# Performance work log

Measured on AMD Instinct MI355X. Metric: run time of the kernel, lower is better.

The kernel has to match this reference:

```python
import jax, jax.numpy as jnp
import numpy as np
from jax import lax

N_GRAPHS = 256
N_NODES = 128      # nodes per graph (fixed-size batching)
N_TPLT = 16
N_TPLT_NODES = 10
N_FEAT = 128
AVG_DEG = 8
EPS = 0.1          # entropic regularization for the GW solver
OUTER_ITERS = 5    # outer mirror-descent (entropic GW) iterations
SINKHORN_ITERS = 20


def setup_inputs() -> dict:
    key = jax.random.key(0)
    k1, k2, k3, k4, k5 = jax.random.split(key, 5)
    x = jax.random.normal(k1, (N_GRAPHS * N_NODES, N_FEAT), jnp.float32)
    # per-graph random edges with global node ids (PyG convention)
    n_e = N_NODES * AVG_DEG
    src = jax.random.randint(k2, (N_GRAPHS, n_e), 0, N_NODES)
    dst = jax.random.randint(k3, (N_GRAPHS, n_e), 0, N_NODES)
    off = (jnp.arange(N_GRAPHS) * N_NODES)[:, None]
    edge_index = jnp.stack([(src + off).reshape(-1), (dst + off).reshape(-1)]).astype(jnp.int32)
    batch = jnp.repeat(jnp.arange(N_GRAPHS, dtype=jnp.int32), N_NODES)
    # template parameters (symmetric uniform adjacencies, normal features, zero q0 -> uniform weights)
    A0 = jax.random.uniform(k4, (N_TPLT, N_TPLT_NODES, N_TPLT_NODES), jnp.float32)
    tplt_adjacencies = 0.5 * (A0 + jnp.swapaxes(A0, 1, 2))
    tplt_features = jax.random.normal(k5, (N_TPLT, N_TPLT_NODES, N_FEAT), jnp.float32)
    q0 = jnp.zeros((N_TPLT, N_TPLT_NODES), jnp.float32)
    return {"x": x, "edge_index": edge_index, "batch": batch,
            "tplt_adjacencies": tplt_adjacencies, "tplt_features": tplt_features, "q0": q0}


def _gw_distances(C1, C2, p, q):
    # C1: [B,N,N] graph adjacencies, C2: [T,M,M] templates, p: [N], q: [T,M]
    # square-loss GW decomposition (Peyre et al.): f1=a^2, f2=b^2, h1=a, h2=2b
    B, N = C1.shape[0], C1.shape[1]
    T, M = C2.shape[0], C2.shape[1]
    f1p = jnp.einsum('bij,j->bi', C1 * C1, p)          # [B,N]
    f2q = jnp.einsum('tij,tj->ti', C2 * C2, q)         # [T,M]
    constC = f1p[:, None, :, None] + f2q[None, :, None, :]  # [B,T,N,M]

    def tens(P):
        # constC - h1(C1) P h2(C2)^T
        cross = jnp.einsum('bik,btkm,tjm->btij', C1, P, 2.0 * C2)
        return constC - cross

    P0 = jnp.broadcast_to(p[None, None, :, None] * q[None, :, None, :], (B, T, N, M))

    def outer(P, _):
        cost = 2.0 * tens(P)                     # GW gradient
        K = jnp.exp(-cost / EPS)                 # [B,T,N,M]
        u0 = jnp.ones((B, T, N), K.dtype)
        v0 = jnp.ones((B, T, M), K.dtype)

        def inner(carry, _):
            u, v = carry
            u = p[None, None, :] / jnp.einsum('btnm,btm->btn', K, v)
            v = q[None, :, :] / jnp.einsum('btnm,btn->btm', K, u)
            return (u, v), None

        (u, v), _ = lax.scan(inner, (u0, v0), None, length=SINKHORN_ITERS)
        P = u[..., :, None] * K * v[..., None, :]
        return P, None

    P, _ = lax.scan(outer, P0, None, length=OUTER_ITERS)
    return jnp.sum(tens(P) * P, axis=(2, 3))     # [B,T]


def reference(x, edge_index, batch, tplt_adjacencies, tplt_features, q0):
    # q = softmax(q0, dim=1): template node weights
    q = jax.nn.softmax(q0, axis=1)
    # dense per-graph adjacency from the sparse edge list
    g = batch[edge_index[0]]
    src = edge_index[0] - g * N_NODES
    dst = edge_index[1] - g * N_NODES
    C1 = jnp.zeros((N_GRAPHS, N_NODES, N_NODES), x.dtype)
    C1 = C1.at[g, src, dst].set(1.0)
    C1 = jnp.maximum(C1, jnp.swapaxes(C1, 1, 2))  # undirected
    p = jnp.full((N_NODES,), 1.0 / N_NODES, x.dtype)  # uniform graph node weights
    # fused=False: pure Gromov-Wasserstein, node features are not used
    return _gw_distances(C1, tplt_adjacencies, p, q)
```

## Files before the change

kernel.cpp:

```cpp
#include <hip/hip_runtime.h>
#include <hip/hip_bf16.h>

#define NGRAPH 256
#define NN     128
#define NT     16
#define NM     10
#define OUTER_IT 5
#define SINK_IT  20
#define COST_SCALE 20.0f

template <int CTRL>
__device__ __forceinline__ float dpp_add(float a) {
  int t = __builtin_amdgcn_update_dpp(0, __float_as_int(a), CTRL, 0xf, 0xf, true);
  return a + __int_as_float(t);
}

__device__ __forceinline__ float wave_allsum(float x) {
  float a = x;
  a = dpp_add<0x111>(a);
  a = dpp_add<0x112>(a);
  a = dpp_add<0x114>(a);
  a = dpp_add<0x118>(a);
  a = dpp_add<0x142>(a);
  a = dpp_add<0x143>(a);
  return __int_as_float(__builtin_amdgcn_readlane(__float_as_int(a), 63));
}

__global__ __launch_bounds__(64, 4)
void tgw_kernel(const int* __restrict__ ei,
                const float* __restrict__ tadj,
                const float* __restrict__ q0g,
                float* __restrict__ out,
                int E, int ne) {
  const int b    = blockIdx.x >> 4;
  const int t    = blockIdx.x & 15;
  const int lane = threadIdx.x;

  __shared__ unsigned adj[NN][4];
  __shared__ __align__(16) float Pls[NN][12];
  __shared__ float C2s[NM][NM];
  __shared__ float q0s[NM];

  unsigned* aflat = &adj[0][0];
  #pragma unroll
  for (int i = 0; i < 8; ++i) aflat[lane + 64 * i] = 0u;

  for (int i = lane; i < NM * NM; i += 64)
    (&C2s[0][0])[i] = tadj[t * NM * NM + i];
  if (lane < NM) q0s[lane] = q0g[t * NM + lane];
  __syncthreads();

  const int* srcp = ei;
  const int* dstp = ei + E;
  const int ebase = b * ne;
  for (int e = lane; e < ne; e += 64) {
    int s = srcp[ebase + e] & (NN - 1);
    int d = dstp[ebase + e] & (NN - 1);
    atomicOr(&adj[s][d >> 5], 1u << (d & 31));
    atomicOr(&adj[d][s >> 5], 1u << (s & 31));
  }
  __syncthreads();

  float qv[NM], f2q[NM];
  {
    float mx = q0s[0];
    #pragma unroll
    for (int j = 1; j < NM; ++j) mx = fmaxf(mx, q0s[j]);
    float s = 0.f;
    #pragma unroll
    for (int j = 0; j < NM; ++j) { qv[j] = __expf(q0s[j] - mx); s += qv[j]; }
    float inv = __builtin_amdgcn_rcpf(s);
    #pragma unroll
    for (int j = 0; j < NM; ++j) qv[j] *= inv;
  }
  #pragma unroll
  for (int j = 0; j < NM; ++j) {
    float a = 0.f;
    #pragma unroll
    for (int m = 0; m < NM; ++m) { float c = C2s[j][m]; a = fmaf(c * c, qv[m], a); }
    f2q[j] = a;
  }

  unsigned long long mk0[2], mk1[2];
  mk0[0] = adj[lane][0]      | ((unsigned long long)adj[lane][1]      << 32);
  mk0[1] = adj[lane][2]      | ((unsigned long long)adj[lane][3]      << 32);
  mk1[0] = adj[lane + 64][0] | ((unsigned long long)adj[lane + 64][1] << 32);
  mk1[1] = adj[lane + 64][2] | ((unsigned long long)adj[lane + 64][3] << 32);
  const float pw = 1.0f / 128.0f;
  float f1p0 = (float)(__popcll(mk0[0]) + __popcll(mk0[1])) * pw;
  float f1p1 = (float)(__popcll(mk1[0]) + __popcll(mk1[1])) * pw;

  #pragma unroll
  for (int j = 0; j < NM; ++j) {
    float pv = qv[j] * pw;
    Pls[lane][j]      = pv;
    Pls[lane + 64][j] = pv;
  }
  __syncthreads();

  auto gather = [&](const unsigned long long* mk, float* S) {
    #pragma unroll
    for (int j = 0; j < NM; ++j) S[j] = 0.f;
    #pragma unroll
    for (int w = 0; w < 2; ++w) {
      unsigned long long bits = mk[w];
      while (bits) {
        int k = (w << 6) + (int)__builtin_ctzll(bits);
        bits &= bits - 1;
        const float* row = Pls[k];
        #pragma unroll
        for (int j = 0; j < NM; ++j) S[j] += row[j];
      }
    }
  };

  float K0[NM], K1[NM], vv[NM];
  float u0 = 0.f, u1 = 0.f;

  for (int o = 0; o < OUTER_IT; ++o) {
    float S0[NM], S1[NM];
    gather(mk0, S0);
    gather(mk1, S1);
    #pragma unroll
    for (int j = 0; j < NM; ++j) {
      float cr0 = 0.f, cr1 = 0.f;
      #pragma unroll
      for (int m = 0; m < NM; ++m) {
        float c = C2s[j][m];
        cr0 = fmaf(S0[m], c, cr0);
        cr1 = fmaf(S1[m], c, cr1);
      }
      float t0 = f1p0 + f2q[j] - 2.f * cr0;
      float t1 = f1p1 + f2q[j] - 2.f * cr1;
      K0[j] = __expf(-COST_SCALE * t0);
      K1[j] = __expf(-COST_SCALE * t1);
    }
    #pragma unroll
    for (int j = 0; j < NM; ++j) vv[j] = 1.f;
    for (int it = 0; it < SINK_IT; ++it) {
      float d0 = 0.f, d1 = 0.f;
      #pragma unroll
      for (int j = 0; j < NM; ++j) { d0 = fmaf(K0[j], vv[j], d0); d1 = fmaf(K1[j], vv[j], d1); }
      u0 = pw * __builtin_amdgcn_rcpf(d0);
      u1 = pw * __builtin_amdgcn_rcpf(d1);
      #pragma unroll
      for (int j = 0; j < NM; ++j) {
        float w  = fmaf(K0[j], u0, K1[j] * u1);
        float cs = wave_allsum(w);
        vv[j] = qv[j] * __builtin_amdgcn_rcpf(cs);
      }
    }
    #pragma unroll
    for (int j = 0; j < NM; ++j) {
      Pls[lane][j]      = u0 * K0[j] * vv[j];
      Pls[lane + 64][j] = u1 * K1[j] * vv[j];
    }
    __syncthreads();
  }

  float S0[NM], S1[NM];
  gather(mk0, S0);
  gather(mk1, S1);
  float acc = 0.f;
  #pragma unroll
  for (int j = 0; j < NM; ++j) {
    float cr0 = 0.f, cr1 = 0.f;
    #pragma unroll
    for (int m = 0; m < NM; ++m) {
      float c = C2s[j][m];
      cr0 = fmaf(S0[m], c, cr0);
      cr1 = fmaf(S1[m], c, cr1);
    }
    float t0 = f1p0 + f2q[j] - 2.f * cr0;
    float t1 = f1p1 + f2q[j] - 2.f * cr1;
    acc += t0 * (u0 * K0[j] * vv[j]) + t1 * (u1 * K1[j] * vv[j]);
  }
  float total = wave_allsum(acc);
  if (lane == 0) out[b * NT + t] = total;
}

extern "C" void kernel_launch(void* const* d_in, const int* in_sizes, int n_in,
                              void* d_out, int out_size, void* d_ws, size_t ws_size,
                              hipStream_t stream) {
  const int* ei    = (const int*)d_in[1];
  const float* c2  = (const float*)d_in[3];
  const float* q0  = (const float*)d_in[5];
  float* out       = (float*)d_out;
  const int E  = in_sizes[1] / 2;
  const int ne = E / NGRAPH;
  tgw_kernel<<<dim3(NGRAPH * NT), dim3(64), 0, stream>>>(ei, c2, q0, out, E, ne);
}
```

Before: 235.0 us.

## Pack four templates per wave with 16-lane groups handling eight rows each

Each 64-lane wave now handles four templates for one graph. Every 16-lane group owns one template and processes 8 node rows per lane, so the Sinkhorn column sums need only a 16-lane DPP reduction with no readlane. The adjacency build is shared across the four templates, and the first outer iteration's gather is replaced by a closed form (degree times q). The grid shrinks by a factor of four and each thread holds far more register state (8x10 K values), which lowers occupancy and leaves fewer blocks to spread over the GPU.

```diff
diff --git a/kernel.cpp b/kernel.cpp
--- a/kernel.cpp
+++ b/kernel.cpp
@@ -1,5 +1,4 @@
 #include <hip/hip_runtime.h>
-#include <hip/hip_bf16.h>
 
 #define NGRAPH 256
 #define NN     128
@@ -9,45 +8,45 @@
 #define SINK_IT  20
 #define COST_SCALE 20.0f
 
+typedef unsigned long long u64;
+
 template <int CTRL>
 __device__ __forceinline__ float dpp_add(float a) {
   int t = __builtin_amdgcn_update_dpp(0, __float_as_int(a), CTRL, 0xf, 0xf, true);
   return a + __int_as_float(t);
 }
-
-__device__ __forceinline__ float wave_allsum(float x) {
-  float a = x;
-  a = dpp_add<0x111>(a);
-  a = dpp_add<0x112>(a);
-  a = dpp_add<0x114>(a);
-  a = dpp_add<0x118>(a);
-  a = dpp_add<0x142>(a);
-  a = dpp_add<0x143>(a);
-  return __int_as_float(__builtin_amdgcn_readlane(__float_as_int(a), 63));
-}
-
-__global__ __launch_bounds__(64, 4)
+__device__ __forceinline__ float allsum16(float x) {
+  x = dpp_add<0xB1>(x);
+  x = dpp_add<0x4E>(x);
+  x = dpp_add<0x141>(x);
+  x = dpp_add<0x140>(x);
+  return x;
+}
+
+__global__ __launch_bounds__(64, 1)
 void tgw_kernel(const int* __restrict__ ei,
                 const float* __restrict__ tadj,
                 const float* __restrict__ q0g,
                 float* __restrict__ out,
                 int E, int ne) {
-  const int b    = blockIdx.x >> 4;
-  const int t    = blockIdx.x & 15;
   const int lane = threadIdx.x;
+  const int g    = lane >> 4;
+  const int sub  = lane & 15;
+  const int b    = blockIdx.x >> 2;
+  const int tb   = (blockIdx.x & 3) * 4;
 
   __shared__ unsigned adj[NN][4];
-  __shared__ __align__(16) float Pls[NN][12];
-  __shared__ float C2s[NM][NM];
-  __shared__ float q0s[NM];
-
-  unsigned* aflat = &adj[0][0];
-  #pragma unroll
-  for (int i = 0; i < 8; ++i) aflat[lane + 64 * i] = 0u;
-
-  for (int i = lane; i < NM * NM; i += 64)
-    (&C2s[0][0])[i] = tadj[t * NM * NM + i];
-  if (lane < NM) q0s[lane] = q0g[t * NM + lane];
+  __shared__ __align__(16) float Pls[4][129][12];
+  __shared__ __align__(16) float C2s[4][NM][12];
+  __shared__ float q0s[4][NM];
+
+  for (int i = lane; i < NN * 4; i += 64) (&adj[0][0])[i] = 0u;
+  for (int i = lane; i < 4 * NM * NM; i += 64) {
+    int tt = i / (NM * NM), rem = i % (NM * NM);
+    C2s[tt][rem / NM][rem % NM] = tadj[(tb + tt) * NM * NM + rem];
+  }
+  for (int i = lane; i < 4 * NM; i += 64)
+    q0s[i / NM][i % NM] = q0g[tb * NM + i];
   __syncthreads();
 
   const int* srcp = ei;
@@ -63,12 +62,12 @@
 
   float qv[NM], f2q[NM];
   {
-    float mx = q0s[0];
-    #pragma unroll
-    for (int j = 1; j < NM; ++j) mx = fmaxf(mx, q0s[j]);
+    float mx = q0s[g][0];
+    #pragma unroll
+    for (int j = 1; j < NM; ++j) mx = fmaxf(mx, q0s[g][j]);
     float s = 0.f;
     #pragma unroll
-    for (int j = 0; j < NM; ++j) { qv[j] = __expf(q0s[j] - mx); s += qv[j]; }
+    for (int j = 0; j < NM; ++j) { qv[j] = __expf(q0s[g][j] - mx); s += qv[j]; }
     float inv = __builtin_amdgcn_rcpf(s);
     #pragma unroll
     for (int j = 0; j < NM; ++j) qv[j] *= inv;
@@ -77,116 +76,162 @@
   for (int j = 0; j < NM; ++j) {
     float a = 0.f;
     #pragma unroll
-    for (int m = 0; m < NM; ++m) { float c = C2s[j][m]; a = fmaf(c * c, qv[m], a); }
+    for (int m = 0; m < NM; ++m) { float c = C2s[g][j][m]; a = fmaf(c * c, qv[m], a); }
     f2q[j] = a;
   }
 
-  unsigned long long mk0[2], mk1[2];
-  mk0[0] = adj[lane][0]      | ((unsigned long long)adj[lane][1]      << 32);
-  mk0[1] = adj[lane][2]      | ((unsigned long long)adj[lane][3]      << 32);
-  mk1[0] = adj[lane + 64][0] | ((unsigned long long)adj[lane + 64][1] << 32);
-  mk1[1] = adj[lane + 64][2] | ((unsigned long long)adj[lane + 64][3] << 32);
   const float pw = 1.0f / 128.0f;
-  float f1p0 = (float)(__popcll(mk0[0]) + __popcll(mk0[1])) * pw;
-  float f1p1 = (float)(__popcll(mk1[0]) + __popcll(mk1[1])) * pw;
-
+  float f1p[8];
   #pragma unroll
-  for (int j = 0; j < NM; ++j) {
-    float pv = qv[j] * pw;
-    Pls[lane][j]      = pv;
-    Pls[lane + 64][j] = pv;
-  }
-  __syncthreads();
-
-  auto gather = [&](const unsigned long long* mk, float* S) {
-    #pragma unroll
-    for (int j = 0; j < NM; ++j) S[j] = 0.f;
-    #pragma unroll
-    for (int w = 0; w < 2; ++w) {
-      unsigned long long bits = mk[w];
-      while (bits) {
-        int k = (w << 6) + (int)__builtin_ctzll(bits);
-        bits &= bits - 1;
-        const float* row = Pls[k];
-        #pragma unroll
-        for (int j = 0; j < NM; ++j) S[j] += row[j];
-      }
+  for (int jj = 0; jj < 8; ++jj) {
+    uint4 mm = *(const uint4*)&adj[sub + 16 * jj][0];
+    u64 m0 = mm.x | ((u64)mm.y << 32), m1 = mm.z | ((u64)mm.w << 32);
+    f1p[jj] = (float)(__popcll(m0) + __popcll(m1)) * pw;
+  }
+
+  auto gather4 = [&](int jj0, float S4[4][NM]) {
+    #pragma unroll
+    for (int c = 0; c < 4; ++c) {
+      const int r = sub + 16 * (jj0 + c);
+      uint4 mm = *(const uint4*)&adj[r][0];
+      u64 m0 = mm.x | ((u64)mm.y << 32), m1 = mm.z | ((u64)mm.w << 32);
+      float S[NM];
+      #pragma unroll
+      for (int j = 0; j < NM; ++j) S[j] = 0.f;
+      while (m0) {
+        int k = (int)__builtin_ctzll(m0); m0 &= m0 - 1;
+        const float* row = &Pls[g][k][0];
+        float4 a = *(const float4*)row;
+        float4 bb = *(const float4*)(row + 4);
+        float2 cc = *(const float2*)(row + 8);
+        S[0] += a.x;  S[1] += a.y;  S[2] += a.z;  S[3] += a.w;
+        S[4] += bb.x; S[5] += bb.y; S[6] += bb.z; S[7] += bb.w;
+        S[8] += cc.x; S[9] += cc.y;
+      }
+      while (m1) {
+        int k = 64 + (int)__builtin_ctzll(m1); m1 &= m1 - 1;
+        const float* row = &Pls[g][k][0];
+        float4 a = *(const float4*)row;
+        float4 bb = *(const float4*)(row + 4);
+        float2 cc = *(const float2*)(row + 8);
+        S[0] += a.x;  S[1] += a.y;  S[2] += a.z;  S[3] += a.w;
+        S[4] += bb.x; S[5] += bb.y; S[6] += bb.z; S[7] += bb.w;
+        S[8] += cc.x; S[9] += cc.y;
+      }
+      #pragma unroll
+      for (int j = 0; j < NM; ++j) S4[c][j] = S[j];
     }
   };
 
-  float K0[NM], K1[NM], vv[NM];
-  float u0 = 0.f, u1 = 0.f;
+  float Kc[8][NM], vv[NM], uu[8];
 
   for (int o = 0; o < OUTER_IT; ++o) {
-    float S0[NM], S1[NM];
-    gather(mk0, S0);
-    gather(mk1, S1);
-    #pragma unroll
-    for (int j = 0; j < NM; ++j) {
-      float cr0 = 0.f, cr1 = 0.f;
-      #pragma unroll
-      for (int m = 0; m < NM; ++m) {
-        float c = C2s[j][m];
-        cr0 = fmaf(S0[m], c, cr0);
-        cr1 = fmaf(S1[m], c, cr1);
-      }
-      float t0 = f1p0 + f2q[j] - 2.f * cr0;
-      float t1 = f1p1 + f2q[j] - 2.f * cr1;
-      K0[j] = __expf(-COST_SCALE * t0);
-      K1[j] = __expf(-COST_SCALE * t1);
-    }
+    #pragma unroll
+    for (int half = 0; half < 2; ++half) {
+      const int jj0 = half * 4;
+      float S4[4][NM];
+      if (o == 0) {
+        #pragma unroll
+        for (int c = 0; c < 4; ++c)
+          #pragma unroll
+          for (int j = 0; j < NM; ++j) S4[c][j] = f1p[jj0 + c] * qv[j];
+      } else {
+        gather4(jj0, S4);
+      }
+      #pragma unroll
+      for (int j = 0; j < NM; ++j) {
+        const float* c2r = &C2s[g][j][0];
+        float4 ca = *(const float4*)c2r;
+        float4 cb = *(const float4*)(c2r + 4);
+        float2 cd = *(const float2*)(c2r + 8);
+        #pragma unroll
+        for (int c = 0; c < 4; ++c) {
+          float cr = S4[c][0] * ca.x;
+          cr = fmaf(S4[c][1], ca.y, cr); cr = fmaf(S4[c][2], ca.z, cr);
+          cr = fmaf(S4[c][3], ca.w, cr); cr = fmaf(S4[c][4], cb.x, cr);
+          cr = fmaf(S4[c][5], cb.y, cr); cr = fmaf(S4[c][6], cb.z, cr);
+          cr = fmaf(S4[c][7], cb.w, cr); cr = fmaf(S4[c][8], cd.x, cr);
+          cr = fmaf(S4[c][9], cd.y, cr);
+          float tv = f1p[jj0 + c] + f2q[j] - 2.f * cr;
+          Kc[jj0 + c][j] = __expf(-COST_SCALE * tv);
+        }
+      }
+    }
+
     #pragma unroll
     for (int j = 0; j < NM; ++j) vv[j] = 1.f;
     for (int it = 0; it < SINK_IT; ++it) {
-      float d0 = 0.f, d1 = 0.f;
-      #pragma unroll
-      for (int j = 0; j < NM; ++j) { d0 = fmaf(K0[j], vv[j], d0); d1 = fmaf(K1[j], vv[j], d1); }
-      u0 = pw * __builtin_amdgcn_rcpf(d0);
-      u1 = pw * __builtin_amdgcn_rcpf(d1);
+      #pragma unroll
+      for (int jj = 0; jj < 8; ++jj) {
+        float d = Kc[jj][0] * vv[0];
+        #pragma unroll
+        for (int j = 1; j < NM; ++j) d = fmaf(Kc[jj][j], vv[j], d);
+        uu[jj] = pw * __builtin_amdgcn_rcpf(d);
+      }
       #pragma unroll
       for (int j = 0; j < NM; ++j) {
-        float w  = fmaf(K0[j], u0, K1[j] * u1);
-        float cs = wave_allsum(w);
+        float w = Kc[0][j] * uu[0];
+        #pragma unroll
+        for (int jj = 1; jj < 8; ++jj) w = fmaf(Kc[jj][j], uu[jj], w);
+        float cs = allsum16(w);
         vv[j] = qv[j] * __builtin_amdgcn_rcpf(cs);
       }
     }
-    #pragma unroll
-    for (int j = 0; j < NM; ++j) {
-      Pls[lane][j]      = u0 * K0[j] * vv[j];
-      Pls[lane + 64][j] = u1 * K1[j] * vv[j];
-    }
+
     __syncthreads();
-  }
-
-  float S0[NM], S1[NM];
-  gather(mk0, S0);
-  gather(mk1, S1);
+    #pragma unroll
+    for (int jj = 0; jj < 8; ++jj) {
+      const int r = sub + 16 * jj;
+      float x[NM];
+      #pragma unroll
+      for (int j = 0; j < NM; ++j) x[j] = uu[jj] * Kc[jj][j] * vv[j];
+      float* row = &Pls[g][r][0];
+      *(float4*)row       = make_float4(x[0], x[1], x[2], x[3]);
+      *(float4*)(row + 4) = make_float4(x[4], x[5], x[6], x[7]);
+      *(float2*)(row + 8) = make_float2(x[8], x[9]);
+    }
+    __syncthreads();
+  }
+
   float acc = 0.f;
   #pragma unroll
-  for (int j = 0; j < NM; ++j) {
-    float cr0 = 0.f, cr1 = 0.f;
-    #pragma unroll
-    for (int m = 0; m < NM; ++m) {
-      float c = C2s[j][m];
-      cr0 = fmaf(S0[m], c, cr0);
-      cr1 = fmaf(S1[m], c, cr1);
-    }
-    float t0 = f1p0 + f2q[j] - 2.f * cr0;
-    float t1 = f1p1 + f2q[j] - 2.f * cr1;
-    acc += t0 * (u0 * K0[j] * vv[j]) + t1 * (u1 * K1[j] * vv[j]);
-  }
-  float total = wave_allsum(acc);
-  if (lane == 0) out[b * NT + t] = total;
+  for (int half = 0; half < 2; ++half) {
+    const int jj0 = half * 4;
+    float S4[4][NM];
+    gather4(jj0, S4);
+    #pragma unroll
+    for (int j = 0; j < NM; ++j) {
+      const float* c2r = &C2s[g][j][0];
+      float4 ca = *(const float4*)c2r;
+      float4 cb = *(const float4*)(c2r + 4);
+      float2 cd = *(const float2*)(c2r + 8);
+      #pragma unroll
+      for (int c = 0; c < 4; ++c) {
+        const int jj = jj0 + c;
+        float cr = S4[c][0] * ca.x;
+        cr = fmaf(S4[c][1], ca.y, cr); cr = fmaf(S4[c][2], ca.z, cr);
+        cr = fmaf(S4[c][3], ca.w, cr); cr = fmaf(S4[c][4], cb.x, cr);
+        cr = fmaf(S4[c][5], cb.y, cr); cr = fmaf(S4[c][6], cb.z, cr);
+        cr = fmaf(S4[c][7], cb.w, cr); cr = fmaf(S4[c][8], cd.x, cr);
+        cr = fmaf(S4[c][9], cd.y, cr);
+        float tv = f1p[jj] + f2q[j] - 2.f * cr;
+        float Pv = uu[jj] * Kc[jj][j] * vv[j];
+        acc = fmaf(tv, Pv, acc);
+      }
+    }
+  }
+  float total = allsum16(acc);
+  if (sub == 0) out[b * NT + tb + g] = total;
 }
 
 extern "C" void kernel_launch(void* const* d_in, const int* in_sizes, int n_in,
                               void* d_out, int out_size, void* d_ws, size_t ws_size,
                               hipStream_t stream) {
-  const int* ei    = (const int*)d_in[1];
-  const float* c2  = (const float*)d_in[3];
-  const float* q0  = (const float*)d_in[5];
-  float* out       = (float*)d_out;
+  const int* ei   = (const int*)d_in[1];
+  const float* c2 = (const float*)d_in[3];
+  const float* q0 = (const float*)d_in[5];
+  float* out      = (float*)d_out;
   const int E  = in_sizes[1] / 2;
   const int ne = E / NGRAPH;
-  tgw_kernel<<<dim3(NGRAPH * NT), dim3(64), 0, stream>>>(ei, c2, q0, out, E, ne);
-}
+  tgw_kernel<<<dim3(NGRAPH * 4), dim3(64), 0, stream>>>(ei, c2, q0, out, E, ne);
+}
```

Measured after the change: 226.9 us. -3.4%, faster.
